# Kernel optimization log

Measured on AMD Instinct MI355X. Metric: run time of the kernel, lower is better.

Reference implementation:

```python
import jax, jax.numpy as jnp
import numpy as np

MARGIN = 1.0


def setup_inputs() -> dict:
    key = jax.random.key(0)
    k1, k2 = jax.random.split(key)
    B, D, K = 2048, 256, 8
    scores = jax.random.normal(k1, (B, D), dtype=jnp.float32)
    pos_indices = jax.random.randint(k2, (B, K), 0, D, dtype=jnp.int64)
    return {"scores": scores, "pos_indices": pos_indices, "num_developers": D}


def reference(scores, pos_indices, num_developers):
    B, D = scores.shape
    # boolean positive mask per sample (duplicate indices collapse like a set)
    pos_mask = jnp.zeros((B, D), dtype=scores.dtype)
    pos_mask = pos_mask.at[jnp.arange(B)[:, None], pos_indices].set(1.0)
    neg_mask = 1.0 - pos_mask
    # all-pairs hinge: relu(s_neg - s_pos + margin), masked to (neg, pos) pairs
    # diff[b, n, p] = scores[b, n] - scores[b, p] + margin
    diff = scores[:, :, None] - scores[:, None, :] + MARGIN
    pair_mask = neg_mask[:, :, None] * pos_mask[:, None, :]
    loss_sum = jnp.sum(jax.nn.relu(diff) * pair_mask)
    num_pairs = jnp.sum(pair_mask)
    # original returns 0.0 when there are no (pos, neg) pairs
    return jnp.where(num_pairs > 0, loss_sum / jnp.maximum(num_pairs, 1.0), 0.0)
```

## Files before the change

kernel.cpp:

```cpp
#include <hip/hip_runtime.h>

#define TPB 256
#define MAXK 64

__global__ __launch_bounds__(TPB) void mlrl_main(
        const float* __restrict__ scores,
        const int* __restrict__ idx,
        const int* __restrict__ ndev,
        int total_scores, int total_idx,
        float2* __restrict__ partials) {
    const int D = *ndev;
    const int B = total_scores / D;
    const int K = total_idx / B;

    __shared__ int   sh_idx[MAXK];
    __shared__ float sh_pos[MAXK];
    __shared__ int   sh_valid[MAXK];

    float loss  = 0.0f;
    float pairs = 0.0f;

    for (int b = blockIdx.x; b < B; b += gridDim.x) {
        const long row = (long)b * D;

        if (threadIdx.x < K) sh_idx[threadIdx.x] = idx[(long)b * K + threadIdx.x];
        __syncthreads();
        if (threadIdx.x < K) {
            const int my = sh_idx[threadIdx.x];
            int valid = 1;
            for (int j = 0; j < (int)threadIdx.x; ++j)
                if (sh_idx[j] == my) valid = 0;
            sh_valid[threadIdx.x] = valid;
            sh_pos[threadIdx.x]   = scores[row + my];
        }
        __syncthreads();

        int P = 0;
        for (int k = 0; k < K; ++k) P += sh_valid[k];

        for (int d = threadIdx.x; d < D; d += blockDim.x) {
            bool is_pos = false;
            for (int k = 0; k < K; ++k) is_pos |= (sh_idx[k] == d);
            if (!is_pos) {
                const float s = scores[row + d] + 1.0f;
                for (int k = 0; k < K; ++k) {
                    if (sh_valid[k]) {
                        float v = s - sh_pos[k];
                        loss += (v > 0.0f) ? v : 0.0f;
                    }
                }
            }
        }
        if (threadIdx.x == 0) pairs += (float)((D - P) * P);
        __syncthreads();
    }

    for (int off = 32; off > 0; off >>= 1) {
        loss  += __shfl_down(loss,  off);
        pairs += __shfl_down(pairs, off);
    }
    __shared__ float2 red[TPB / 64];
    const int wave = threadIdx.x >> 6;
    const int lane = threadIdx.x & 63;
    if (lane == 0) red[wave] = make_float2(loss, pairs);
    __syncthreads();
    if (threadIdx.x == 0) {
        float2 acc = red[0];
        for (int w = 1; w < TPB / 64; ++w) { acc.x += red[w].x; acc.y += red[w].y; }
        partials[blockIdx.x] = acc;
    }
}

__global__ __launch_bounds__(TPB) void mlrl_finalize(
        const float2* __restrict__ partials, int n, float* __restrict__ out) {
    double l = 0.0, p = 0.0;
    for (int i = threadIdx.x; i < n; i += blockDim.x) {
        float2 v = partials[i];
        l += (double)v.x;
        p += (double)v.y;
    }
    for (int off = 32; off > 0; off >>= 1) {
        l += __shfl_down(l, off);
        p += __shfl_down(p, off);
    }
    __shared__ double sl[TPB / 64], sp[TPB / 64];
    const int wave = threadIdx.x >> 6;
    const int lane = threadIdx.x & 63;
    if (lane == 0) { sl[wave] = l; sp[wave] = p; }
    __syncthreads();
    if (threadIdx.x == 0) {
        double L = 0.0, P = 0.0;
        for (int w = 0; w < TPB / 64; ++w) { L += sl[w]; P += sp[w]; }
        out[0] = (P > 0.0) ? (float)(L / (P < 1.0 ? 1.0 : P)) : 0.0f;
    }
}

extern "C" void kernel_launch(void* const* d_in, const int* in_sizes, int n_in,
                              void* d_out, int out_size, void* d_ws, size_t ws_size,
                              hipStream_t stream) {
    const float* scores = (const float*)d_in[0];
    const int*   idx    = (const int*)d_in[1];
    const int*   ndev   = (const int*)d_in[2];
    float* out = (float*)d_out;

    const int total_scores = in_sizes[0];
    const int total_idx    = in_sizes[1];

    int nblocks = total_scores / 256;
    if (nblocks < 1) nblocks = 1;
    size_t need = (size_t)nblocks * sizeof(float2);
    if (need > ws_size) nblocks = (int)(ws_size / sizeof(float2));

    float2* partials = (float2*)d_ws;

    mlrl_main<<<nblocks, TPB, 0, stream>>>(scores, idx, ndev,
                                           total_scores, total_idx, partials);
    mlrl_finalize<<<1, TPB, 0, stream>>>(partials, nblocks, out);
}
```

Before: 66.57 us.

## Fuse finalize into main kernel via last-block atomic counter, specialize K=8 in registers

Merges the two kernels into one, where the last block to finish, detected through an atomic counter, performs the final reduction. A hipMemsetAsync resets the counter on each call. The K=8 path is templated, so positive indices and scores live in registers instead of shared memory, and the per-sample __syncthreads barriers go away. The grid is fixed at 512 blocks instead of B, so each block now processes several samples. The aim is to remove a kernel launch and the shared-memory barriers, at the cost of an extra memset and the serialized tail of the last block.

```diff
diff --git a/kernel.cpp b/kernel.cpp
--- a/kernel.cpp
+++ b/kernel.cpp
@@ -1,65 +1,98 @@
 #include <hip/hip_runtime.h>
 
 #define TPB 256
-#define MAXK 64
+#define NBLK 512
 
-__global__ __launch_bounds__(TPB) void mlrl_main(
+template <int KC>
+__device__ inline void accum_samples(const float* __restrict__ scores,
+                                     const int* __restrict__ idx,
+                                     int D, int B, int K,
+                                     float& loss, float& pairs) {
+    const int KK = (KC > 0) ? KC : K;
+    for (int b = blockIdx.x; b < B; b += gridDim.x) {
+        const int rbase = b * D;
+        const int ibase = b * K;
+
+        if (KC > 0) {
+            int   ik[KC > 0 ? KC : 1];
+            float ps[KC > 0 ? KC : 1];
+            int   validmask = 0, P = 0;
+#pragma unroll
+            for (int k = 0; k < KC; ++k) ik[k] = idx[ibase + k];
+#pragma unroll
+            for (int k = 0; k < KC; ++k) {
+                bool dup = false;
+#pragma unroll
+                for (int j = 0; j < KC; ++j)
+                    if (j < k) dup |= (ik[j] == ik[k]);
+                if (!dup) { validmask |= (1 << k); ++P; }
+                ps[k] = scores[rbase + ik[k]];
+            }
+            for (int d = threadIdx.x; d < D; d += TPB) {
+                const float s = scores[rbase + d] + 1.0f;
+                bool is_pos = false;
+#pragma unroll
+                for (int k = 0; k < KC; ++k) is_pos |= (ik[k] == d);
+                if (!is_pos) {
+#pragma unroll
+                    for (int k = 0; k < KC; ++k) {
+                        if (validmask & (1 << k)) {
+                            float v = s - ps[k];
+                            loss += (v > 0.0f) ? v : 0.0f;
+                        }
+                    }
+                }
+            }
+            if (threadIdx.x == 0) pairs += (float)((D - P) * P);
+        } else {
+            int P = 0;
+            for (int k = 0; k < KK; ++k) {
+                bool dup = false;
+                for (int j = 0; j < k; ++j) dup |= (idx[ibase + j] == idx[ibase + k]);
+                if (!dup) ++P;
+            }
+            for (int d = threadIdx.x; d < D; d += TPB) {
+                const float s = scores[rbase + d] + 1.0f;
+                bool is_pos = false;
+                for (int k = 0; k < KK; ++k) is_pos |= (idx[ibase + k] == d);
+                if (!is_pos) {
+                    for (int k = 0; k < KK; ++k) {
+                        bool dup = false;
+                        for (int j = 0; j < k; ++j) dup |= (idx[ibase + j] == idx[ibase + k]);
+                        if (!dup) {
+                            float v = s - scores[rbase + idx[ibase + k]];
+                            loss += (v > 0.0f) ? v : 0.0f;
+                        }
+                    }
+                }
+            }
+            if (threadIdx.x == 0) pairs += (float)((D - P) * P);
+        }
+    }
+}
+
+__global__ __launch_bounds__(TPB) void mlrl_fused(
         const float* __restrict__ scores,
         const int* __restrict__ idx,
         const int* __restrict__ ndev,
         int total_scores, int total_idx,
-        float2* __restrict__ partials) {
+        unsigned int* __restrict__ counter,
+        float2* __restrict__ partials,
+        float* __restrict__ out) {
     const int D = *ndev;
     const int B = total_scores / D;
     const int K = total_idx / B;
 
-    __shared__ int   sh_idx[MAXK];
-    __shared__ float sh_pos[MAXK];
-    __shared__ int   sh_valid[MAXK];
-
-    float loss  = 0.0f;
-    float pairs = 0.0f;
-
-    for (int b = blockIdx.x; b < B; b += gridDim.x) {
-        const long row = (long)b * D;
-
-        if (threadIdx.x < K) sh_idx[threadIdx.x] = idx[(long)b * K + threadIdx.x];
-        __syncthreads();
-        if (threadIdx.x < K) {
-            const int my = sh_idx[threadIdx.x];
-            int valid = 1;
-            for (int j = 0; j < (int)threadIdx.x; ++j)
-                if (sh_idx[j] == my) valid = 0;
-            sh_valid[threadIdx.x] = valid;
-            sh_pos[threadIdx.x]   = scores[row + my];
-        }
-        __syncthreads();
-
-        int P = 0;
-        for (int k = 0; k < K; ++k) P += sh_valid[k];
-
-        for (int d = threadIdx.x; d < D; d += blockDim.x) {
-            bool is_pos = false;
-            for (int k = 0; k < K; ++k) is_pos |= (sh_idx[k] == d);
-            if (!is_pos) {
-                const float s = scores[row + d] + 1.0f;
-                for (int k = 0; k < K; ++k) {
-                    if (sh_valid[k]) {
-                        float v = s - sh_pos[k];
-                        loss += (v > 0.0f) ? v : 0.0f;
-                    }
-                }
-            }
-        }
-        if (threadIdx.x == 0) pairs += (float)((D - P) * P);
-        __syncthreads();
-    }
+    float loss = 0.0f, pairs = 0.0f;
+    if (K == 8) accum_samples<8>(scores, idx, D, B, K, loss, pairs);
+    else        accum_samples<0>(scores, idx, D, B, K, loss, pairs);
 
     for (int off = 32; off > 0; off >>= 1) {
         loss  += __shfl_down(loss,  off);
         pairs += __shfl_down(pairs, off);
     }
     __shared__ float2 red[TPB / 64];
+    __shared__ bool   amLast;
     const int wave = threadIdx.x >> 6;
     const int lane = threadIdx.x & 63;
     if (lane == 0) red[wave] = make_float2(loss, pairs);
@@ -68,30 +101,32 @@
         float2 acc = red[0];
         for (int w = 1; w < TPB / 64; ++w) { acc.x += red[w].x; acc.y += red[w].y; }
         partials[blockIdx.x] = acc;
+        __threadfence();
+        unsigned int old = atomicAdd(counter, 1u);
+        amLast = (old == (unsigned int)gridDim.x - 1u);
     }
-}
+    __syncthreads();
 
-__global__ __launch_bounds__(TPB) void mlrl_finalize(
-        const float2* __restrict__ partials, int n, float* __restrict__ out) {
-    double l = 0.0, p = 0.0;
-    for (int i = threadIdx.x; i < n; i += blockDim.x) {
-        float2 v = partials[i];
-        l += (double)v.x;
-        p += (double)v.y;
-    }
-    for (int off = 32; off > 0; off >>= 1) {
-        l += __shfl_down(l, off);
-        p += __shfl_down(p, off);
-    }
-    __shared__ double sl[TPB / 64], sp[TPB / 64];
-    const int wave = threadIdx.x >> 6;
-    const int lane = threadIdx.x & 63;
-    if (lane == 0) { sl[wave] = l; sp[wave] = p; }
-    __syncthreads();
-    if (threadIdx.x == 0) {
-        double L = 0.0, P = 0.0;
-        for (int w = 0; w < TPB / 64; ++w) { L += sl[w]; P += sp[w]; }
-        out[0] = (P > 0.0) ? (float)(L / (P < 1.0 ? 1.0 : P)) : 0.0f;
+    if (amLast) {
+        __threadfence();
+        double l = 0.0, p = 0.0;
+        for (int i = threadIdx.x; i < (int)gridDim.x; i += TPB) {
+            float2 v = partials[i];
+            l += (double)v.x;
+            p += (double)v.y;
+        }
+        for (int off = 32; off > 0; off >>= 1) {
+            l += __shfl_down(l, off);
+            p += __shfl_down(p, off);
+        }
+        __shared__ double sl[TPB / 64], sp[TPB / 64];
+        if (lane == 0) { sl[wave] = l; sp[wave] = p; }
+        __syncthreads();
+        if (threadIdx.x == 0) {
+            double L = 0.0, P = 0.0;
+            for (int w = 0; w < TPB / 64; ++w) { L += sl[w]; P += sp[w]; }
+            out[0] = (P > 0.0) ? (float)(L / (P < 1.0 ? 1.0 : P)) : 0.0f;
+        }
     }
 }
 
@@ -106,14 +141,12 @@
     const int total_scores = in_sizes[0];
     const int total_idx    = in_sizes[1];
 
-    int nblocks = total_scores / 256;
-    if (nblocks < 1) nblocks = 1;
-    size_t need = (size_t)nblocks * sizeof(float2);
-    if (need > ws_size) nblocks = (int)(ws_size / sizeof(float2));
+    unsigned int* counter  = (unsigned int*)d_ws;
+    float2*       partials = (float2*)((char*)d_ws + 16);
 
-    float2* partials = (float2*)d_ws;
+    hipMemsetAsync(d_ws, 0, 4, stream);
 
-    mlrl_main<<<nblocks, TPB, 0, stream>>>(scores, idx, ndev,
-                                           total_scores, total_idx, partials);
-    mlrl_finalize<<<1, TPB, 0, stream>>>(partials, nblocks, out);
+    mlrl_fused<<<NBLK, TPB, 0, stream>>>(scores, idx, ndev,
+                                         total_scores, total_idx,
+                                         counter, partials, out);
 }
```

Result: slower. 74.59 us (+12.1%).
